# Kernel tuning notes

Hardware: AMD Instinct MI355X
Metric: run time of the kernel (lower is better)

The kernel has to match this reference:

```python
import jax, jax.numpy as jnp
import numpy as np
from jax import lax

EPS = 2e-5      # BatchNorm eps from source
TCLIP = 1.3     # FastSign STE clip


def fast_sign(x):
    # forward: sign(x); backward: grad of clamp(x, -1.3, 1.3) (straight-through)
    c = jnp.clip(x, -TCLIP, TCLIP)
    return lax.stop_gradient(jnp.sign(x) - c) + c


def conv2d(x, w, b, stride, pad):
    y = lax.conv_general_dilated(
        x, w, window_strides=stride,
        padding=[(pad[0], pad[0]), (pad[1], pad[1])],
        dimension_numbers=('NCHW', 'OIHW', 'NCHW'))
    return y + b[None, :, None, None]


def batchnorm(x, g, b):
    # training-mode BN: biased batch stats over (N, H, W)
    m = jnp.mean(x, axis=(0, 2, 3), keepdims=True)
    v = jnp.var(x, axis=(0, 2, 3), keepdims=True)
    return g[None, :, None, None] * (x - m) * lax.rsqrt(v + EPS) + b[None, :, None, None]


def maxpool3x3s2(x):
    return lax.reduce_window(x, -jnp.inf, lax.max, (1, 1, 3, 3), (1, 1, 2, 2), 'VALID')


def setup_inputs() -> dict:
    key = jax.random.key(0)
    ks = jax.random.split(key, 16)
    s = 0.05
    rn = lambda k, shape: jax.random.normal(k, shape, dtype=jnp.float32) * s
    NUM_CLASSES = 1000
    return {
        'x': jax.random.normal(ks[0], (8, 3, 211, 211), dtype=jnp.float32),
        'conv1_w': rn(ks[1], (96, 3, 11, 11)), 'conv1_b': rn(ks[2], (96,)),
        'bn1_g': jnp.ones((96,), jnp.float32), 'bn1_b': jnp.zeros((96,), jnp.float32),
        'conv2_w': rn(ks[3], (256, 96, 5, 5)), 'conv2_b': rn(ks[4], (256,)),
        'bn2_g': jnp.ones((256,), jnp.float32), 'bn2_b': jnp.zeros((256,), jnp.float32),
        'conv3_w': rn(ks[5], (384, 256, 3, 3)), 'conv3_b': rn(ks[6], (384,)),
        'bn3_g': jnp.ones((384,), jnp.float32), 'bn3_b': jnp.zeros((384,), jnp.float32),
        'conv4_w': rn(ks[7], (384, 384, 3, 3)), 'conv4_b': rn(ks[8], (384,)),
        'bn4_g': jnp.ones((384,), jnp.float32), 'bn4_b': jnp.zeros((384,), jnp.float32),
        'conv5_w': rn(ks[9], (256, 384, 3, 3)), 'conv5_b': rn(ks[10], (256,)),
        'bn5_g': jnp.ones((256,), jnp.float32), 'bn5_b': jnp.zeros((256,), jnp.float32),
        'fc1_w': rn(ks[11], (4096, 5)),
        'bn6_g': jnp.ones((256,), jnp.float32), 'bn6_b': jnp.zeros((256,), jnp.float32),
        'fc2_w': rn(ks[12], (4096, 4096)),
        'bn7_g': jnp.ones((256,), jnp.float32), 'bn7_b': jnp.zeros((256,), jnp.float32),
        'fc3_w': rn(ks[13], (NUM_CLASSES, 4096)), 'fc3_b': rn(ks[14], (NUM_CLASSES,)),
    }


def reference(x, conv1_w, conv1_b, bn1_g, bn1_b,
              conv2_w, conv2_b, bn2_g, bn2_b,
              conv3_w, conv3_b, bn3_g, bn3_b,
              conv4_w, conv4_b, bn4_g, bn4_b,
              conv5_w, conv5_b, bn5_g, bn5_b,
              fc1_w, bn6_g, bn6_b,
              fc2_w, bn7_g, bn7_b,
              fc3_w, fc3_b):
    # conv1 (full precision) + BN + relu + pool
    x = conv2d(x, conv1_w, conv1_b, (4, 4), (0, 0))           # [B,96,51,51]
    x = jax.nn.relu(batchnorm(x, bn1_g, bn1_b))
    x = maxpool3x3s2(x)                                        # [B,96,25,25]
    # binary conv blocks (act_q then BinaryConv2d binarizes input again, as in torch)
    x = fast_sign(x)
    x = conv2d(fast_sign(x), fast_sign(conv2_w), conv2_b, (1, 1), (2, 2))  # [B,256,25,25]
    x = batchnorm(x, bn2_g, bn2_b)
    x = maxpool3x3s2(x)                                        # [B,256,12,12]
    x = fast_sign(x)
    x = conv2d(fast_sign(x), fast_sign(conv3_w), conv3_b, (1, 1), (1, 1))  # [B,384,12,12]
    x = batchnorm(x, bn3_g, bn3_b)
    x = fast_sign(x)
    x = conv2d(fast_sign(x), fast_sign(conv4_w), conv4_b, (1, 1), (1, 1))
    x = batchnorm(x, bn4_g, bn4_b)
    x = fast_sign(x)
    x = conv2d(fast_sign(x), fast_sign(conv5_w), conv5_b, (1, 1), (1, 1))  # [B,256,12,12]
    x = batchnorm(x, bn5_g, bn5_b)
    x = maxpool3x3s2(x)                                        # [B,256,5,5]
    # fc layers applied on the LAST dim of the 4D tensor (faithful to torch F.linear)
    x = fast_sign(x)
    x = jnp.matmul(fast_sign(x), fast_sign(fc1_w).T)           # [B,256,5,4096]
    x = jax.nn.relu(batchnorm(x, bn6_g, bn6_b))
    x = fast_sign(x)
    x = jnp.matmul(fast_sign(x), fast_sign(fc2_w).T)           # [B,256,5,4096]
    x = jax.nn.relu(batchnorm(x, bn7_g, bn7_b))
    x = jnp.matmul(x, fc3_w.T) + fc3_b                         # [B,256,5,1000]
    return jax.nn.softmax(x, axis=1)                           # softmax over dim=1 (channels)
```

## Files before the change

kernel.cpp:

```cpp
#include <hip/hip_runtime.h>
#include <cstdint>
#include <cstddef>


typedef int      v4i  __attribute__((ext_vector_type(4)));
typedef float    v4f  __attribute__((ext_vector_type(4)));
typedef _Float16 v8h  __attribute__((ext_vector_type(8)));

#define EPS_BN 2e-5

__device__ __forceinline__ void g2l16(const void* g, void* l) {
  __builtin_amdgcn_global_load_lds((__attribute__((address_space(1))) void*)g,
                                   (__attribute__((address_space(3))) void*)l,
                                   16, 0, 0);
}

__global__ __launch_bounds__(256) void conv1_k(const float* __restrict__ x,
                                               const float* __restrict__ w,
                                               float* __restrict__ y) {
  const int bid = blockIdx.x;
  const int n = bid / 51, oh = bid % 51;
  const int tid = threadIdx.x, lane = tid & 63, wave = tid >> 6;
  __shared__ __align__(16) float xs[3 * 11 * 272];
  for (int i = tid; i < 3 * 11 * 272; i += 256) {
    int iw = i % 272;
    int t = i / 272;
    int kh = t % 11, ci = t / 11;
    float v = 0.f;
    if (iw < 211) v = x[((size_t)(n * 3 + ci) * 211 + (oh * 4 + kh)) * 211 + iw];
    xs[i] = v;
  }
  __syncthreads();
  const int ow = lane;
  const int g = blockIdx.y;
  {
    const int co0 = wave * 24 + g * 4;
    float a0 = 0.f, a1 = 0.f, a2 = 0.f, a3 = 0.f;
    for (int ci = 0; ci < 3; ++ci) {
#pragma unroll
      for (int kh = 0; kh < 11; ++kh) {
        const float* xr = xs + (ci * 11 + kh) * 272 + ow * 4;
        float4 q0 = *(const float4*)(xr);
        float4 q1 = *(const float4*)(xr + 4);
        float4 q2 = *(const float4*)(xr + 8);
        float xv[11] = {q0.x, q0.y, q0.z, q0.w, q1.x, q1.y,
                        q1.z, q1.w, q2.x, q2.y, q2.z};
        const float* wr = w + ((size_t)co0 * 3 + ci) * 121 + kh * 11;
#pragma unroll
        for (int kw = 0; kw < 11; ++kw) {
          float xvv = xv[kw];
          a0 = fmaf(xvv, wr[kw], a0);
          a1 = fmaf(xvv, wr[363 + kw], a1);
          a2 = fmaf(xvv, wr[726 + kw], a2);
          a3 = fmaf(xvv, wr[1089 + kw], a3);
        }
      }
    }
    if (ow < 51) {
      size_t ob = ((size_t)(n * 96 + co0) * 51 + oh) * 51 + ow;
      y[ob] = a0;
      y[ob + 2601] = a1;
      y[ob + 2 * 2601] = a2;
      y[ob + 3 * 2601] = a3;
    }
  }
}

template <typename T>
__global__ __launch_bounds__(256) void bnstat_nchw_k(const T* __restrict__ y,
                                                     const float* __restrict__ g,
                                                     const float* __restrict__ bb,
                                                     float* __restrict__ par,
                                                     int C, int HW, int Nn) {
  const int c = blockIdx.x;
  double s = 0.0, q = 0.0;
  for (int n = 0; n < Nn; ++n) {
    const T* p = y + ((size_t)n * C + c) * HW;
    for (int r = threadIdx.x; r < HW; r += 256) {
      double v = (double)p[r];
      s += v;
      q += v * v;
    }
  }
  __shared__ double ss[256], qq[256];
  ss[threadIdx.x] = s;
  qq[threadIdx.x] = q;
  __syncthreads();
  for (int st = 128; st > 0; st >>= 1) {
    if (threadIdx.x < st) {
      ss[threadIdx.x] += ss[threadIdx.x + st];
      qq[threadIdx.x] += qq[threadIdx.x + st];
    }
    __syncthreads();
  }
  if (threadIdx.x == 0) {
    double P = (double)Nn * HW;
    double m = ss[0] / P, var = qq[0] / P - m * m;
    float inv = (float)(1.0 / sqrt(var + EPS_BN));
    float sc = g[c] * inv;
    par[c] = sc;
    par[512 + c] = bb[c] - (float)m * sc;
  }
}

template <typename T>
__global__ __launch_bounds__(256) void bnstat_nhwc_k(const T* __restrict__ y,
                                                     const float* __restrict__ g,
                                                     const float* __restrict__ bb,
                                                     float* __restrict__ par,
                                                     int C, int P) {
  const int c = blockIdx.x;
  double s = 0.0, q = 0.0;
  for (int p = threadIdx.x; p < P; p += 256) {
    double v = (double)y[(size_t)p * C + c];
    s += v;
    q += v * v;
  }
  __shared__ double ss[256], qq[256];
  ss[threadIdx.x] = s;
  qq[threadIdx.x] = q;
  __syncthreads();
  for (int st = 128; st > 0; st >>= 1) {
    if (threadIdx.x < st) {
      ss[threadIdx.x] += ss[threadIdx.x + st];
      qq[threadIdx.x] += qq[threadIdx.x + st];
    }
    __syncthreads();
  }
  if (threadIdx.x == 0) {
    double Pd = (double)P;
    double m = ss[0] / Pd, var = qq[0] / Pd - m * m;
    float inv = (float)(1.0 / sqrt(var + EPS_BN));
    float sc = g[c] * inv;
    par[c] = sc;
    par[512 + c] = bb[c] - (float)m * sc;
  }
}

__global__ __launch_bounds__(256) void bnp16_k(const short* __restrict__ y,
                                               double* __restrict__ part) {
  const int c = blockIdx.x, n = blockIdx.y;
  const short* p = y + ((size_t)(n * 256 + c)) * 20480;
  long long s = 0, q = 0;
  for (int r = threadIdx.x; r < 20480; r += 256) {
    int v = p[r];
    s += v;
    q += (long long)v * v;
  }
  __shared__ long long ss[256], qq[256];
  ss[threadIdx.x] = s;
  qq[threadIdx.x] = q;
  __syncthreads();
  for (int st = 128; st > 0; st >>= 1) {
    if (threadIdx.x < st) {
      ss[threadIdx.x] += ss[threadIdx.x + st];
      qq[threadIdx.x] += qq[threadIdx.x + st];
    }
    __syncthreads();
  }
  if (threadIdx.x == 0) {
    part[(size_t)(n * 256 + c) * 2] = (double)ss[0];
    part[(size_t)(n * 256 + c) * 2 + 1] = (double)qq[0];
  }
}

__global__ __launch_bounds__(256) void bnf7_k(const double* __restrict__ part,
                                              const float* __restrict__ g,
                                              const float* __restrict__ bb,
                                              float* __restrict__ par) {
  int c = threadIdx.x;
  double s = 0.0, q = 0.0;
  for (int n = 0; n < 8; ++n) {
    s += part[(size_t)(n * 256 + c) * 2];
    q += part[(size_t)(n * 256 + c) * 2 + 1];
  }
  double P = 163840.0;
  double m = s / P, var = q / P - m * m;
  float inv = (float)(1.0 / sqrt(var + EPS_BN));
  float sc = g[c] * inv;
  par[c] = sc;
  par[512 + c] = bb[c] - (float)m * sc;
}

__global__ __launch_bounds__(256) void pool1sign_k(const float* __restrict__ y,
                                                   const float* __restrict__ par,
                                                   int8_t* __restrict__ o) {
  unsigned idx = blockIdx.x * 256 + threadIdx.x;
  if (idx >= 8u * 96 * 25 * 25) return;
  unsigned ow = idx % 25, t = idx / 25;
  unsigned oh = t % 25;
  t /= 25;
  unsigned c = t % 96, n = t / 96;
  float sc = par[c], sh = par[512 + c];
  const float* p = y + ((size_t)(n * 96 + c) * 51 + oh * 2) * 51 + ow * 2;
  float mx = -1e30f, mn = 1e30f;
#pragma unroll
  for (int kh = 0; kh < 3; ++kh)
#pragma unroll
    for (int kw = 0; kw < 3; ++kw) {
      float v = p[kh * 51 + kw];
      mx = fmaxf(mx, v);
      mn = fminf(mn, v);
    }
  float z = (sc >= 0.f ? sc * mx : sc * mn) + sh;
  o[((n * 25 + oh) * 25 + ow) * 96 + c] = (z > 0.f) ? 1 : 0;
}

__global__ __launch_bounds__(256) void poolsign_k(const short* __restrict__ y,
                                                  const float* __restrict__ par,
                                                  int8_t* __restrict__ o, int Nn,
                                                  int Hin, int C, int Hout) {
  unsigned idx = blockIdx.x * 256 + threadIdx.x;
  if (idx >= (unsigned)Nn * Hout * Hout * C) return;
  unsigned c = idx % C;
  unsigned t = idx / C;
  unsigned ow = t % Hout;
  t /= Hout;
  unsigned oh = t % Hout;
  unsigned n = t / Hout;
  const short* p = y + ((size_t)(n * Hin + oh * 2) * Hin + ow * 2) * C + c;
  int mx = -1000000, mn = 1000000;
#pragma unroll
  for (int kh = 0; kh < 3; ++kh)
#pragma unroll
    for (int kw = 0; kw < 3; ++kw) {
      int v = p[(kh * Hin + kw) * C];
      mx = max(mx, v);
      mn = min(mn, v);
    }
  float sc = par[c];
  float z = (sc >= 0.f ? sc * (float)mx : sc * (float)mn) + par[512 + c];
  o[idx] = (z > 0.f) ? 1 : ((z < 0.f) ? -1 : 0);
}

__global__ __launch_bounds__(256) void signk(const short* __restrict__ y,
                                             const float* __restrict__ par,
                                             int8_t* __restrict__ o, int total,
                                             int C) {
  unsigned idx = blockIdx.x * 256 + threadIdx.x;
  if (idx >= (unsigned)total) return;
  unsigned c = idx % C;
  float z = par[c] * (float)y[idx] + par[512 + c];
  o[idx] = (z > 0.f) ? 1 : ((z < 0.f) ? -1 : 0);
}

__global__ __launch_bounds__(256) void pool5sign_k(const short* __restrict__ y,
                                                   const float* __restrict__ par,
                                                   int8_t* __restrict__ o) {
  unsigned idx = blockIdx.x * 256 + threadIdx.x;
  if (idx >= 8u * 256 * 25) return;
  unsigned ow = idx % 5;
  unsigned t = idx / 5;
  unsigned oh = t % 5;
  t /= 5;
  unsigned c = t % 256, n = t / 256;
  const short* p = y + ((size_t)(n * 12 + oh * 2) * 12 + ow * 2) * 256 + c;
  int mx = -1000000, mn = 1000000;
#pragma unroll
  for (int kh = 0; kh < 3; ++kh)
#pragma unroll
    for (int kw = 0; kw < 3; ++kw) {
      int v = p[(kh * 12 + kw) * 256];
      mx = max(mx, v);
      mn = min(mn, v);
    }
  float sc = par[c];
  float z = (sc >= 0.f ? sc * (float)mx : sc * (float)mn) + par[512 + c];
  o[idx] = (z > 0.f) ? 1 : ((z < 0.f) ? -1 : 0);
}

__global__ __launch_bounds__(256) void quantw_k(const float* __restrict__ w,
                                                int8_t* __restrict__ o, int Co,
                                                int Ci, int KHW, int K, int Kp) {
  unsigned idx = blockIdx.x * 256 + threadIdx.x;
  if (idx >= (unsigned)Co * Kp) return;
  unsigned k = idx % Kp;
  unsigned co = idx / Kp;
  int8_t v = 0;
  if (k < (unsigned)K) {
    unsigned tap = k / Ci, ci = k - tap * Ci;
    float f = w[((size_t)co * Ci + ci) * KHW + tap];
    v = (f > 0.f) ? 1 : ((f < 0.f) ? -1 : 0);
  }
  o[idx] = v;
}

__global__ __launch_bounds__(256) void quantwv_k(const float* __restrict__ w,
                                                 int8_t* __restrict__ o,
                                                 unsigned total4) {
  unsigned idx = blockIdx.x * 256 + threadIdx.x;
  if (idx >= total4) return;
  float4 f = ((const float4*)w)[idx];
  union { int8_t b[4]; int i; } u;
  u.b[0] = (f.x > 0.f) ? 1 : ((f.x < 0.f) ? -1 : 0);
  u.b[1] = (f.y > 0.f) ? 1 : ((f.y < 0.f) ? -1 : 0);
  u.b[2] = (f.z > 0.f) ? 1 : ((f.z < 0.f) ? -1 : 0);
  u.b[3] = (f.w > 0.f) ? 1 : ((f.w < 0.f) ? -1 : 0);
  ((int*)o)[idx] = u.i;
}

__global__ __launch_bounds__(256) void im2colv_k(const int8_t* __restrict__ a,
                                                 int8_t* __restrict__ o, int Nn,
                                                 int H, int C, int KH, int pad,
                                                 int K, int Kp) {
  unsigned t = blockIdx.x * 256 + threadIdx.x;
  unsigned chunks = (unsigned)Kp >> 4;
  unsigned total = (unsigned)Nn * H * H * chunks;
  if (t >= total) return;
  unsigned kc = t % chunks;
  unsigned m = t / chunks;
  unsigned ow = m % H;
  unsigned tmp = m / H;
  unsigned oh = tmp % H;
  unsigned n = tmp / H;
  unsigned k0 = kc << 4;
  int4 v = {0, 0, 0, 0};
  if (k0 < (unsigned)K) {
    unsigned tap = k0 / C;
    unsigned ci = k0 - tap * C;
    unsigned kh = tap / KH, kw = tap - kh * KH;
    int ih = (int)oh - pad + (int)kh, iw = (int)ow - pad + (int)kw;
    if (ih >= 0 && ih < H && iw >= 0 && iw < H)
      v = *(const int4*)(a + (((n * H + ih) * H + iw) * C + ci));
  }
  *(int4*)(o + (size_t)m * Kp + k0) = v;
}

__global__ __launch_bounds__(256) void gemm_i8_k(const int8_t* __restrict__ A,
                                                 const int8_t* __restrict__ B,
                                                 short* __restrict__ Cm, int M,
                                                 int N, int Kp) {
  __shared__ __align__(16) int8_t As[128 * 64];
  __shared__ __align__(16) int8_t Bs[128 * 64];
  const int tid = threadIdx.x;
  const int lane = tid & 63, wave = tid >> 6;
  const int m0 = blockIdx.x * 128, n0 = blockIdx.y * 128;
  const int wm = (wave >> 1) * 64, wn = (wave & 1) * 64;
  v4i acc[4][4];
#pragma unroll
  for (int r = 0; r < 4; ++r)
#pragma unroll
    for (int u = 0; u < 4; ++u) acc[r][u] = (v4i){0, 0, 0, 0};

  int r_[2], g_[2];
#pragma unroll
  for (int q = 0; q < 2; ++q) {
    int idx = q * 256 + tid;
    r_[q] = idx >> 2;
    g_[q] = (((idx & 3) ^ ((r_[q] >> 1) & 3)) << 4);
  }
  int aoff[4], boff[4];
#pragma unroll
  for (int r = 0; r < 4; ++r) {
    int m = wm + r * 16 + (lane & 15);
    aoff[r] = m * 64 + (((lane >> 4) ^ ((m >> 1) & 3)) << 4);
    int n = wn + r * 16 + (lane & 15);
    boff[r] = n * 64 + (((lane >> 4) ^ ((n >> 1) & 3)) << 4);
  }

  for (int k0 = 0; k0 < Kp; k0 += 64) {
#pragma unroll
    for (int q = 0; q < 2; ++q) {
      int idx = q * 256 + tid;
      g2l16(A + (size_t)(m0 + r_[q]) * Kp + k0 + g_[q], As + idx * 16);
      g2l16(B + (size_t)(n0 + r_[q]) * Kp + k0 + g_[q], Bs + idx * 16);
    }
    __syncthreads();
    v4i af[4], bf[4];
#pragma unroll
    for (int r = 0; r < 4; ++r) {
      af[r] = *(const v4i*)(As + aoff[r]);
      bf[r] = *(const v4i*)(Bs + boff[r]);
    }
#pragma unroll
    for (int r = 0; r < 4; ++r)
#pragma unroll
      for (int u = 0; u < 4; ++u)
        acc[r][u] = __builtin_amdgcn_mfma_i32_16x16x64_i8(af[r], bf[u],
                                                          acc[r][u], 0, 0, 0);
    __syncthreads();
  }
  const int colD = lane & 15, rowD = (lane >> 4) * 4;
#pragma unroll
  for (int r = 0; r < 4; ++r)
#pragma unroll
    for (int u = 0; u < 4; ++u) {
      int n = n0 + wn + u * 16 + colD;
#pragma unroll
      for (int e = 0; e < 4; ++e) {
        int m = m0 + wm + r * 16 + rowD + e;
        if (m < M) Cm[(size_t)m * N + n] = (short)acc[r][u][e];
      }
    }
}

__global__ __launch_bounds__(256) void gemm_i8_64k(const int8_t* __restrict__ A,
                                                   const int8_t* __restrict__ B,
                                                   short* __restrict__ Cm, int M,
                                                   int N, int Kp) {
  __shared__ __align__(16) int8_t As[64 * 64];
  __shared__ __align__(16) int8_t Bs[64 * 64];
  const int tid = threadIdx.x;
  const int lane = tid & 63, wave = tid >> 6;
  const int m0 = blockIdx.x * 64, n0 = blockIdx.y * 64;
  const int wm = (wave >> 1) * 32, wn = (wave & 1) * 32;
  v4i acc[2][2];
#pragma unroll
  for (int r = 0; r < 2; ++r)
#pragma unroll
    for (int u = 0; u < 2; ++u) acc[r][u] = (v4i){0, 0, 0, 0};

  const int rs = tid >> 2;
  const int gsw = (((tid & 3) ^ ((rs >> 1) & 3)) << 4);
  int aoff[2], boff[2];
#pragma unroll
  for (int r = 0; r < 2; ++r) {
    int m = wm + r * 16 + (lane & 15);
    aoff[r] = m * 64 + (((lane >> 4) ^ ((m >> 1) & 3)) << 4);
    int n = wn + r * 16 + (lane & 15);
    boff[r] = n * 64 + (((lane >> 4) ^ ((n >> 1) & 3)) << 4);
  }

  for (int k0 = 0; k0 < Kp; k0 += 64) {
    g2l16(A + (size_t)(m0 + rs) * Kp + k0 + gsw, As + tid * 16);
    g2l16(B + (size_t)(n0 + rs) * Kp + k0 + gsw, Bs + tid * 16);
    __syncthreads();
    v4i af[2], bf[2];
#pragma unroll
    for (int r = 0; r < 2; ++r) {
      af[r] = *(const v4i*)(As + aoff[r]);
      bf[r] = *(const v4i*)(Bs + boff[r]);
    }
#pragma unroll
    for (int r = 0; r < 2; ++r)
#pragma unroll
      for (int u = 0; u < 2; ++u)
        acc[r][u] = __builtin_amdgcn_mfma_i32_16x16x64_i8(af[r], bf[u],
                                                          acc[r][u], 0, 0, 0);
    __syncthreads();
  }
  const int colD = lane & 15, rowD = (lane >> 4) * 4;
#pragma unroll
  for (int r = 0; r < 2; ++r)
#pragma unroll
    for (int u = 0; u < 2; ++u) {
      int n = n0 + wn + u * 16 + colD;
#pragma unroll
      for (int e = 0; e < 4; ++e) {
        int m = m0 + wm + r * 16 + rowD + e;
        if (m < M) Cm[(size_t)m * N + n] = (short)acc[r][u][e];
      }
    }
}

__global__ __launch_bounds__(256) void gemm_f16_k(const _Float16* __restrict__ A,
                                                  const _Float16* __restrict__ B,
                                                  float* __restrict__ out,
                                                  const float* __restrict__ bias,
                                                  int M, int Nout, int K) {
  __shared__ __align__(16) int8_t As[128 * 64];
  __shared__ __align__(16) int8_t Bs[128 * 64];
  const int tid = threadIdx.x;
  const int lane = tid & 63, wave = tid >> 6;
  const int m0 = blockIdx.x * 128, n0 = blockIdx.y * 128;
  const int wm = (wave >> 1) * 64, wn = (wave & 1) * 64;
  const int KpB = K * 2;
  v4f acc[4][4];
#pragma unroll
  for (int r = 0; r < 4; ++r)
#pragma unroll
    for (int u = 0; u < 4; ++u) acc[r][u] = (v4f){0.f, 0.f, 0.f, 0.f};

  int r_[2], g_[2];
#pragma unroll
  for (int q = 0; q < 2; ++q) {
    int idx = q * 256 + tid;
    r_[q] = idx >> 2;
    g_[q] = (((idx & 3) ^ ((r_[q] >> 1) & 3)) << 4);
  }
  int aoff[4], boff[4];
#pragma unroll
  for (int r = 0; r < 4; ++r) {
    int m = wm + r * 16 + (lane & 15);
    aoff[r] = m * 64 + (((lane >> 4) ^ ((m >> 1) & 3)) << 4);
    int n = wn + r * 16 + (lane & 15);
    boff[r] = n * 64 + (((lane >> 4) ^ ((n >> 1) & 3)) << 4);
  }

  const int8_t* Ab = (const int8_t*)A;
  const int8_t* Bb = (const int8_t*)B;
  for (int k0 = 0; k0 < KpB; k0 += 64) {
#pragma unroll
    for (int q = 0; q < 2; ++q) {
      int idx = q * 256 + tid;
      g2l16(Ab + (size_t)(m0 + r_[q]) * KpB + k0 + g_[q], As + idx * 16);
      g2l16(Bb + (size_t)(n0 + r_[q]) * KpB + k0 + g_[q], Bs + idx * 16);
    }
    __syncthreads();
    v8h af[4], bf[4];
#pragma unroll
    for (int r = 0; r < 4; ++r) {
      af[r] = *(const v8h*)(As + aoff[r]);
      bf[r] = *(const v8h*)(Bs + boff[r]);
    }
#pragma unroll
    for (int r = 0; r < 4; ++r)
#pragma unroll
      for (int u = 0; u < 4; ++u)
        acc[r][u] = __builtin_amdgcn_mfma_f32_16x16x32_f16(af[r], bf[u],
                                                           acc[r][u], 0, 0, 0);
    __syncthreads();
  }
  const int colD = lane & 15, rowD = (lane >> 4) * 4;
#pragma unroll
  for (int r = 0; r < 4; ++r)
#pragma unroll
    for (int u = 0; u < 4; ++u) {
      int n = n0 + wn + u * 16 + colD;
      if (n < Nout) {
        float bv = bias[n];
#pragma unroll
        for (int e = 0; e < 4; ++e) {
          int m = m0 + wm + r * 16 + rowD + e;
          if (m < M) out[(size_t)m * Nout + n] = acc[r][u][e] + bv;
        }
      }
    }
}

__global__ __launch_bounds__(256) void gram_k(const int8_t* __restrict__ wq1,
                                              int* __restrict__ gm) {
  __shared__ int sg[30];
  if (threadIdx.x < 30) sg[threadIdx.x] = 0;
  __syncthreads();
  int acc[30];
#pragma unroll
  for (int i = 0; i < 30; ++i) acc[i] = 0;
  for (int j = threadIdx.x; j < 4096; j += 256) {
    const int8_t* w = wq1 + j * 5;
    int v[5];
#pragma unroll
    for (int k = 0; k < 5; ++k) v[k] = w[k];
#pragma unroll
    for (int k = 0; k < 5; ++k) {
      acc[k] += v[k];
#pragma unroll
      for (int l = 0; l < 5; ++l) acc[5 + k * 5 + l] += v[k] * v[l];
    }
  }
#pragma unroll
  for (int i = 0; i < 30; ++i) atomicAdd(&sg[i], acc[i]);
  __syncthreads();
  if (threadIdx.x < 30) gm[threadIdx.x] = sg[threadIdx.x];
}

__global__ __launch_bounds__(256) void par6_k(const int8_t* __restrict__ s5,
                                              const int* __restrict__ gm,
                                              const float* __restrict__ g,
                                              const float* __restrict__ bb,
                                              float* __restrict__ par) {
  int c = threadIdx.x;
  long long s = 0, q = 0;
  for (int n = 0; n < 8; ++n)
    for (int i = 0; i < 5; ++i) {
      const int8_t* a = s5 + ((size_t)((n * 256 + c) * 5 + i)) * 5;
      int av[5];
#pragma unroll
      for (int k = 0; k < 5; ++k) av[k] = a[k];
      int ds = 0, dq = 0;
#pragma unroll
      for (int k = 0; k < 5; ++k) {
        ds += av[k] * gm[k];
#pragma unroll
        for (int l = 0; l < 5; ++l) dq += av[k] * av[l] * gm[5 + k * 5 + l];
      }
      s += ds;
      q += dq;
    }
  double P = 163840.0;
  double m = (double)s / P, var = (double)q / P - m * m;
  float inv = (float)(1.0 / sqrt(var + EPS_BN));
  float sc = g[c] * inv;
  par[c] = sc;
  par[512 + c] = bb[c] - (float)m * sc;
}

__global__ __launch_bounds__(256) void fc1f_k(const int8_t* __restrict__ s5,
                                              const int8_t* __restrict__ wq1,
                                              const float* __restrict__ par,
                                              int8_t* __restrict__ f1) {
  unsigned idx = blockIdx.x * 256 + threadIdx.x;
  if (idx >= 10240u * 256) return;
  unsigned m = idx >> 8, jg = idx & 255;
  unsigned c = (m / 5) & 255;
  float sc = par[c], sh = par[512 + c];
  const int8_t* ap = s5 + m * 5;
  int a0 = ap[0], a1 = ap[1], a2 = ap[2], a3 = ap[3], a4 = ap[4];
  int8_t wb[80];
  const int4* wp = (const int4*)(wq1 + jg * 80);
#pragma unroll
  for (int qq = 0; qq < 5; ++qq) *(int4*)(wb + qq * 16) = wp[qq];
  union { int8_t b[16]; int4 v; } ov;
#pragma unroll
  for (int t = 0; t < 16; ++t) {
    int d = a0 * wb[t * 5] + a1 * wb[t * 5 + 1] + a2 * wb[t * 5 + 2] +
            a3 * wb[t * 5 + 3] + a4 * wb[t * 5 + 4];
    float z = sc * (float)d + sh;
    ov.b[t] = (z > 0.f) ? 1 : 0;
  }
  *(int4*)(f1 + (size_t)m * 4096 + jg * 16) = ov.v;
}

__global__ __launch_bounds__(256) void x7v_k(short* __restrict__ f2,
                                             const float* __restrict__ par) {
  unsigned idx = blockIdx.x * 256 + threadIdx.x;
  if (idx >= 10240u * 4096 / 8) return;
  unsigned base8 = idx * 8;
  unsigned c = (base8 / 20480) & 255;
  float sc = par[c], sh = par[512 + c];
  union { int4 v; short s[8]; } in;
  in.v = *(int4*)(f2 + (size_t)base8);
  union { int4 v; _Float16 h[8]; } outv;
#pragma unroll
  for (int t = 0; t < 8; ++t) {
    float z = sc * (float)in.s[t] + sh;
    if (z < 0.f) z = 0.f;
    outv.h[t] = (_Float16)z;
  }
  *(int4*)((_Float16*)f2 + (size_t)base8) = outv.v;
}

__global__ __launch_bounds__(256) void w3h_k(const float* __restrict__ w,
                                             _Float16* __restrict__ o) {
  unsigned idx = blockIdx.x * 256 + threadIdx.x;
  if (idx >= 1024u * 4096) return;
  unsigned j = idx >> 12;
  o[idx] = (j < 1000) ? (_Float16)w[idx] : (_Float16)0.f;
}

__global__ __launch_bounds__(256) void softmax_k(float* __restrict__ o) {
  unsigned t = blockIdx.x * 256 + threadIdx.x;
  if (t >= 40000) return;
  unsigned j = t % 1000;
  unsigned i = (t / 1000) % 5;
  unsigned b = t / 5000;
  float* p = o + ((size_t)(b * 256) * 5 + i) * 1000 + j;
  float mx = -1e30f;
  for (int c = 0; c < 256; ++c) mx = fmaxf(mx, p[(size_t)c * 5000]);
  float s = 0.f;
  for (int c = 0; c < 256; ++c) s += expf(p[(size_t)c * 5000] - mx);
  float inv = 1.f / s;
  for (int c = 0; c < 256; ++c)
    p[(size_t)c * 5000] = expf(p[(size_t)c * 5000] - mx) * inv;
}

static inline unsigned gs(size_t n) { return (unsigned)((n + 255) / 256); }

extern "C" void kernel_launch(void* const* d_in, const int* in_sizes, int n_in,
                              void* d_out, int out_size, void* d_ws,
                              size_t ws_size, hipStream_t stream) {
  (void)in_sizes; (void)n_in; (void)out_size; (void)ws_size;
  const float* x    = (const float*)d_in[0];
  const float* w1   = (const float*)d_in[1];
  const float* bn1g = (const float*)d_in[3];
  const float* bn1b = (const float*)d_in[4];
  const float* w2   = (const float*)d_in[5];
  const float* bn2g = (const float*)d_in[7];
  const float* bn2b = (const float*)d_in[8];
  const float* w3   = (const float*)d_in[9];
  const float* bn3g = (const float*)d_in[11];
  const float* bn3b = (const float*)d_in[12];
  const float* w4   = (const float*)d_in[13];
  const float* bn4g = (const float*)d_in[15];
  const float* bn4b = (const float*)d_in[16];
  const float* w5   = (const float*)d_in[17];
  const float* bn5g = (const float*)d_in[19];
  const float* bn5b = (const float*)d_in[20];
  const float* fc1w = (const float*)d_in[21];
  const float* bn6g = (const float*)d_in[22];
  const float* bn6b = (const float*)d_in[23];
  const float* fc2w = (const float*)d_in[24];
  const float* bn7g = (const float*)d_in[25];
  const float* bn7b = (const float*)d_in[26];
  const float* fc3w = (const float*)d_in[27];
  const float* fc3b = (const float*)d_in[28];
  float* out = (float*)d_out;

  char* ws = (char*)d_ws;
  size_t off = 0;
  auto alloc = [&](size_t bytes) -> void* {
    off = (off + 255) & ~(size_t)255;
    void* p = ws + off;
    off += bytes;
    return p;
  };
  float*   Y1   = (float*)alloc((size_t)8 * 96 * 51 * 51 * 4);
  int8_t*  S1   = (int8_t*)alloc((size_t)8 * 25 * 25 * 96);
  int8_t*  IM   = (int8_t*)alloc((size_t)5120 * 2432);
  short*   Y2   = (short*)alloc((size_t)5056 * 256 * 2);
  int8_t*  S2   = (int8_t*)alloc((size_t)1152 * 256);
  short*   Y3   = (short*)alloc((size_t)1152 * 384 * 2);
  int8_t*  S3   = (int8_t*)alloc((size_t)1152 * 384);
  short*   Y4   = (short*)alloc((size_t)1152 * 384 * 2);
  int8_t*  S4   = (int8_t*)alloc((size_t)1152 * 384);
  short*   Y5   = (short*)alloc((size_t)1152 * 256 * 2);
  int8_t*  S5   = (int8_t*)alloc((size_t)8 * 256 * 25);
  int8_t*  WQ2  = (int8_t*)alloc((size_t)256 * 2432);
  int8_t*  WQ3  = (int8_t*)alloc((size_t)384 * 2304);
  int8_t*  WQ4  = (int8_t*)alloc((size_t)384 * 3456);
  int8_t*  WQ5  = (int8_t*)alloc((size_t)256 * 3456);
  int8_t*  WQ1  = (int8_t*)alloc((size_t)4096 * 5);
  int8_t*  WQF2 = (int8_t*)alloc((size_t)4096 * 4096);
  int8_t*  F1   = (int8_t*)alloc((size_t)10240 * 4096);
  short*   F2   = (short*)alloc((size_t)10240 * 4096 * 2);
  _Float16* W3H = (_Float16*)alloc((size_t)1024 * 4096 * 2);
  float*   PAR  = (float*)alloc((size_t)7 * 1024 * 4);
  int*     GM   = (int*)alloc(32 * 4);
  double*  PART = (double*)alloc((size_t)2048 * 2 * 8);
  float* par1 = PAR;
  float* par2 = PAR + 1024;
  float* par3 = PAR + 2048;
  float* par4 = PAR + 3072;
  float* par5 = PAR + 4096;
  float* par6 = PAR + 5120;
  float* par7 = PAR + 6144;

  quantw_k<<<gs((size_t)256 * 2432), 256, 0, stream>>>(w2, WQ2, 256, 96, 25, 2400, 2432);
  quantw_k<<<gs((size_t)384 * 2304), 256, 0, stream>>>(w3, WQ3, 384, 256, 9, 2304, 2304);
  quantw_k<<<gs((size_t)384 * 3456), 256, 0, stream>>>(w4, WQ4, 384, 384, 9, 3456, 3456);
  quantw_k<<<gs((size_t)256 * 3456), 256, 0, stream>>>(w5, WQ5, 256, 384, 9, 3456, 3456);
  quantw_k<<<gs((size_t)4096 * 5), 256, 0, stream>>>(fc1w, WQ1, 4096, 5, 1, 5, 5);
  quantwv_k<<<gs((size_t)4096 * 1024), 256, 0, stream>>>(fc2w, WQF2, 4096u * 1024);
  w3h_k<<<gs((size_t)1024 * 4096), 256, 0, stream>>>(fc3w, W3H);

  conv1_k<<<dim3(8 * 51, 6), 256, 0, stream>>>(x, w1, Y1);
  bnstat_nchw_k<float><<<dim3(96), 256, 0, stream>>>(Y1, bn1g, bn1b, par1, 96, 2601, 8);
  pool1sign_k<<<gs((size_t)8 * 96 * 625), 256, 0, stream>>>(Y1, par1, S1);

  im2colv_k<<<gs((size_t)5000 * 152), 256, 0, stream>>>(S1, IM, 8, 25, 96, 5, 2, 2400, 2432);
  gemm_i8_64k<<<dim3(79, 4), 256, 0, stream>>>(IM, WQ2, Y2, 5000, 256, 2432);
  bnstat_nhwc_k<short><<<dim3(256), 256, 0, stream>>>(Y2, bn2g, bn2b, par2, 256, 5000);
  poolsign_k<<<gs((size_t)8 * 144 * 256), 256, 0, stream>>>(Y2, par2, S2, 8, 25, 256, 12);

  im2colv_k<<<gs((size_t)1152 * 144), 256, 0, stream>>>(S2, IM, 8, 12, 256, 3, 1, 2304, 2304);
  gemm_i8_64k<<<dim3(18, 6), 256, 0, stream>>>(IM, WQ3, Y3, 1152, 384, 2304);
  bnstat_nhwc_k<short><<<dim3(384), 256, 0, stream>>>(Y3, bn3g, bn3b, par3, 384, 1152);
  signk<<<gs((size_t)1152 * 384), 256, 0, stream>>>(Y3, par3, S3, 1152 * 384, 384);

  im2colv_k<<<gs((size_t)1152 * 216), 256, 0, stream>>>(S3, IM, 8, 12, 384, 3, 1, 3456, 3456);
  gemm_i8_64k<<<dim3(18, 6), 256, 0, stream>>>(IM, WQ4, Y4, 1152, 384, 3456);
  bnstat_nhwc_k<short><<<dim3(384), 256, 0, stream>>>(Y4, bn4g, bn4b, par4, 384, 1152);
  signk<<<gs((size_t)1152 * 384), 256, 0, stream>>>(Y4, par4, S4, 1152 * 384, 384);

  im2colv_k<<<gs((size_t)1152 * 216), 256, 0, stream>>>(S4, IM, 8, 12, 384, 3, 1, 3456, 3456);
  gemm_i8_64k<<<dim3(18, 4), 256, 0, stream>>>(IM, WQ5, Y5, 1152, 256, 3456);
  bnstat_nhwc_k<short><<<dim3(256), 256, 0, stream>>>(Y5, bn5g, bn5b, par5, 256, 1152);
  pool5sign_k<<<gs((size_t)8 * 256 * 25), 256, 0, stream>>>(Y5, par5, S5);

  gram_k<<<dim3(1), 256, 0, stream>>>(WQ1, GM);
  par6_k<<<dim3(1), 256, 0, stream>>>(S5, GM, bn6g, bn6b, par6);
  fc1f_k<<<gs((size_t)10240 * 256), 256, 0, stream>>>(S5, WQ1, par6, F1);

  gemm_i8_k<<<dim3(80, 32), 256, 0, stream>>>(F1, WQF2, F2, 10240, 4096, 4096);
  bnp16_k<<<dim3(256, 8), 256, 0, stream>>>(F2, PART);
  bnf7_k<<<dim3(1), 256, 0, stream>>>(PART, bn7g, bn7b, par7);
  x7v_k<<<gs((size_t)10240 * 512), 256, 0, stream>>>(F2, par7);

  gemm_f16_k<<<dim3(80, 8), 256, 0, stream>>>((const _Float16*)F2, W3H, out, fc3b,
                                              10240, 1000, 4096);
  softmax_k<<<gs(40000), 256, 0, stream>>>(out);
}
```

Measured before the change: 1.099 ms.

## Widen GEMM N tiles to 256 and restructure softmax via shared-memory tiles

Both the int8 fc2 GEMM and the f16 fc3 GEMM now use 128x256 block tiles, each wave owning 64x128, which doubles accumulator registers and B-tile LDS. The aim is more MFMA work per A-tile load and half as many blocks. Separately, softmax is rewritten so each block stages a 256x32 channel tile in LDS and does block-cooperative max and sum reductions, instead of each thread making three strided global passes over 256 channels. The larger accumulator footprint may cut occupancy or cause register spills, and with 1000 outputs the fc3 GEMM wastes more padded columns in its last tile.

```diff
diff --git a/kernel.cpp b/kernel.cpp
--- a/kernel.cpp
+++ b/kernel.cpp
@@ -331,31 +331,35 @@
                                                  short* __restrict__ Cm, int M,
                                                  int N, int Kp) {
   __shared__ __align__(16) int8_t As[128 * 64];
-  __shared__ __align__(16) int8_t Bs[128 * 64];
+  __shared__ __align__(16) int8_t Bs[256 * 64];
   const int tid = threadIdx.x;
   const int lane = tid & 63, wave = tid >> 6;
-  const int m0 = blockIdx.x * 128, n0 = blockIdx.y * 128;
-  const int wm = (wave >> 1) * 64, wn = (wave & 1) * 64;
-  v4i acc[4][4];
+  const int m0 = blockIdx.x * 128, n0 = blockIdx.y * 256;
+  const int wm = (wave >> 1) * 64, wn = (wave & 1) * 128;
+  v4i acc[4][8];
 #pragma unroll
   for (int r = 0; r < 4; ++r)
 #pragma unroll
-    for (int u = 0; u < 4; ++u) acc[r][u] = (v4i){0, 0, 0, 0};
-
-  int r_[2], g_[2];
-#pragma unroll
-  for (int q = 0; q < 2; ++q) {
+    for (int u = 0; u < 8; ++u) acc[r][u] = (v4i){0, 0, 0, 0};
+
+  int r_[6], g_[6];
+#pragma unroll
+  for (int q = 0; q < 6; ++q) {
     int idx = q * 256 + tid;
-    r_[q] = idx >> 2;
-    g_[q] = (((idx & 3) ^ ((r_[q] >> 1) & 3)) << 4);
-  }
-  int aoff[4], boff[4];
+    int row = idx >> 2;
+    r_[q] = (q < 2) ? row : (row - 128);
+    g_[q] = (((idx & 3) ^ ((row >> 1) & 3)) << 4);
+  }
+  int aoff[4], boff[8];
 #pragma unroll
   for (int r = 0; r < 4; ++r) {
     int m = wm + r * 16 + (lane & 15);
     aoff[r] = m * 64 + (((lane >> 4) ^ ((m >> 1) & 3)) << 4);
-    int n = wn + r * 16 + (lane & 15);
-    boff[r] = n * 64 + (((lane >> 4) ^ ((n >> 1) & 3)) << 4);
+  }
+#pragma unroll
+  for (int u = 0; u < 8; ++u) {
+    int n = wn + u * 16 + (lane & 15);
+    boff[u] = n * 64 + (((lane >> 4) ^ ((n >> 1) & 3)) << 4);
   }
 
   for (int k0 = 0; k0 < Kp; k0 += 64) {
@@ -363,19 +367,22 @@
     for (int q = 0; q < 2; ++q) {
       int idx = q * 256 + tid;
       g2l16(A + (size_t)(m0 + r_[q]) * Kp + k0 + g_[q], As + idx * 16);
-      g2l16(B + (size_t)(n0 + r_[q]) * Kp + k0 + g_[q], Bs + idx * 16);
+    }
+#pragma unroll
+    for (int q = 2; q < 6; ++q) {
+      int idx = q * 256 + tid;
+      g2l16(B + (size_t)(n0 + r_[q]) * Kp + k0 + g_[q], Bs + (idx - 512) * 16);
     }
     __syncthreads();
-    v4i af[4], bf[4];
-#pragma unroll
-    for (int r = 0; r < 4; ++r) {
-      af[r] = *(const v4i*)(As + aoff[r]);
-      bf[r] = *(const v4i*)(Bs + boff[r]);
-    }
+    v4i af[4], bf[8];
+#pragma unroll
+    for (int r = 0; r < 4; ++r) af[r] = *(const v4i*)(As + aoff[r]);
+#pragma unroll
+    for (int u = 0; u < 8; ++u) bf[u] = *(const v4i*)(Bs + boff[u]);
 #pragma unroll
     for (int r = 0; r < 4; ++r)
 #pragma unroll
-      for (int u = 0; u < 4; ++u)
+      for (int u = 0; u < 8; ++u)
         acc[r][u] = __builtin_amdgcn_mfma_i32_16x16x64_i8(af[r], bf[u],
                                                           acc[r][u], 0, 0, 0);
     __syncthreads();
@@ -384,7 +391,7 @@
 #pragma unroll
   for (int r = 0; r < 4; ++r)
 #pragma unroll
-    for (int u = 0; u < 4; ++u) {
+    for (int u = 0; u < 8; ++u) {
       int n = n0 + wn + u * 16 + colD;
 #pragma unroll
       for (int e = 0; e < 4; ++e) {
@@ -459,32 +466,36 @@
                                                   const float* __restrict__ bias,
                                                   int M, int Nout, int K) {
   __shared__ __align__(16) int8_t As[128 * 64];
-  __shared__ __align__(16) int8_t Bs[128 * 64];
+  __shared__ __align__(16) int8_t Bs[256 * 64];
   const int tid = threadIdx.x;
   const int lane = tid & 63, wave = tid >> 6;
-  const int m0 = blockIdx.x * 128, n0 = blockIdx.y * 128;
-  const int wm = (wave >> 1) * 64, wn = (wave & 1) * 64;
+  const int m0 = blockIdx.x * 128, n0 = blockIdx.y * 256;
+  const int wm = (wave >> 1) * 64, wn = (wave & 1) * 128;
   const int KpB = K * 2;
-  v4f acc[4][4];
+  v4f acc[4][8];
 #pragma unroll
   for (int r = 0; r < 4; ++r)
 #pragma unroll
-    for (int u = 0; u < 4; ++u) acc[r][u] = (v4f){0.f, 0.f, 0.f, 0.f};
-
-  int r_[2], g_[2];
-#pragma unroll
-  for (int q = 0; q < 2; ++q) {
+    for (int u = 0; u < 8; ++u) acc[r][u] = (v4f){0.f, 0.f, 0.f, 0.f};
+
+  int r_[6], g_[6];
+#pragma unroll
+  for (int q = 0; q < 6; ++q) {
     int idx = q * 256 + tid;
-    r_[q] = idx >> 2;
-    g_[q] = (((idx & 3) ^ ((r_[q] >> 1) & 3)) << 4);
-  }
-  int aoff[4], boff[4];
+    int row = idx >> 2;
+    r_[q] = (q < 2) ? row : (row - 128);
+    g_[q] = (((idx & 3) ^ ((row >> 1) & 3)) << 4);
+  }
+  int aoff[4], boff[8];
 #pragma unroll
   for (int r = 0; r < 4; ++r) {
     int m = wm + r * 16 + (lane & 15);
     aoff[r] = m * 64 + (((lane >> 4) ^ ((m >> 1) & 3)) << 4);
-    int n = wn + r * 16 + (lane & 15);
-    boff[r] = n * 64 + (((lane >> 4) ^ ((n >> 1) & 3)) << 4);
+  }
+#pragma unroll
+  for (int u = 0; u < 8; ++u) {
+    int n = wn + u * 16 + (lane & 15);
+    boff[u] = n * 64 + (((lane >> 4) ^ ((n >> 1) & 3)) << 4);
   }
 
   const int8_t* Ab = (const int8_t*)A;
@@ -494,19 +505,22 @@
     for (int q = 0; q < 2; ++q) {
       int idx = q * 256 + tid;
       g2l16(Ab + (size_t)(m0 + r_[q]) * KpB + k0 + g_[q], As + idx * 16);
-      g2l16(Bb + (size_t)(n0 + r_[q]) * KpB + k0 + g_[q], Bs + idx * 16);
+    }
+#pragma unroll
+    for (int q = 2; q < 6; ++q) {
+      int idx = q * 256 + tid;
+      g2l16(Bb + (size_t)(n0 + r_[q]) * KpB + k0 + g_[q], Bs + (idx - 512) * 16);
     }
     __syncthreads();
-    v8h af[4], bf[4];
-#pragma unroll
-    for (int r = 0; r < 4; ++r) {
-      af[r] = *(const v8h*)(As + aoff[r]);
-      bf[r] = *(const v8h*)(Bs + boff[r]);
-    }
+    v8h af[4], bf[8];
+#pragma unroll
+    for (int r = 0; r < 4; ++r) af[r] = *(const v8h*)(As + aoff[r]);
+#pragma unroll
+    for (int u = 0; u < 8; ++u) bf[u] = *(const v8h*)(Bs + boff[u]);
 #pragma unroll
     for (int r = 0; r < 4; ++r)
 #pragma unroll
-      for (int u = 0; u < 4; ++u)
+      for (int u = 0; u < 8; ++u)
         acc[r][u] = __builtin_amdgcn_mfma_f32_16x16x32_f16(af[r], bf[u],
                                                            acc[r][u], 0, 0, 0);
     __syncthreads();
@@ -515,7 +529,7 @@
 #pragma unroll
   for (int r = 0; r < 4; ++r)
 #pragma unroll
-    for (int u = 0; u < 4; ++u) {
+    for (int u = 0; u < 8; ++u) {
       int n = n0 + wn + u * 16 + colD;
       if (n < Nout) {
         float bv = bias[n];
@@ -639,19 +653,52 @@
 }
 
 __global__ __launch_bounds__(256) void softmax_k(float* __restrict__ o) {
-  unsigned t = blockIdx.x * 256 + threadIdx.x;
-  if (t >= 40000) return;
-  unsigned j = t % 1000;
-  unsigned i = (t / 1000) % 5;
-  unsigned b = t / 5000;
-  float* p = o + ((size_t)(b * 256) * 5 + i) * 1000 + j;
-  float mx = -1e30f;
-  for (int c = 0; c < 256; ++c) mx = fmaxf(mx, p[(size_t)c * 5000]);
-  float s = 0.f;
-  for (int c = 0; c < 256; ++c) s += expf(p[(size_t)c * 5000] - mx);
-  float inv = 1.f / s;
-  for (int c = 0; c < 256; ++c)
-    p[(size_t)c * 5000] = expf(p[(size_t)c * 5000] - mx) * inv;
+  __shared__ float tile[256][33];
+  __shared__ float red[8][32];
+  __shared__ float mxs[32], invs[32];
+  const int bi = blockIdx.x;
+  const int jt = blockIdx.y;
+  const int b = bi / 5, i = bi % 5;
+  float* base = o + ((size_t)(b * 256) * 5 + i) * 1000;
+  const int t = threadIdx.x;
+  const int jl = t & 31, part = t >> 5;
+  const int j = jt * 32 + jl;
+  const bool ok = (j < 1000);
+  for (int cg = 0; cg < 32; ++cg) {
+    int c = cg * 8 + part;
+    tile[c][jl] = ok ? base[(size_t)c * 5000 + j] : 0.f;
+  }
+  __syncthreads();
+  float pm = -1e30f;
+#pragma unroll 4
+  for (int cc = 0; cc < 32; ++cc) pm = fmaxf(pm, tile[part * 32 + cc][jl]);
+  red[part][jl] = pm;
+  __syncthreads();
+  if (part == 0) {
+    float m = red[0][jl];
+#pragma unroll
+    for (int p = 1; p < 8; ++p) m = fmaxf(m, red[p][jl]);
+    mxs[jl] = m;
+  }
+  __syncthreads();
+  float mx = mxs[jl];
+  float ps = 0.f;
+#pragma unroll 4
+  for (int cc = 0; cc < 32; ++cc) ps += expf(tile[part * 32 + cc][jl] - mx);
+  red[part][jl] = ps;
+  __syncthreads();
+  if (part == 0) {
+    float s = red[0][jl];
+#pragma unroll
+    for (int p = 1; p < 8; ++p) s += red[p][jl];
+    invs[jl] = 1.f / s;
+  }
+  __syncthreads();
+  float inv = invs[jl];
+  for (int cg = 0; cg < 32; ++cg) {
+    int c = cg * 8 + part;
+    if (ok) base[(size_t)c * 5000 + j] = expf(tile[c][jl] - mx) * inv;
+  }
 }
 
 static inline unsigned gs(size_t n) { return (unsigned)((n + 255) / 256); }
@@ -761,12 +808,12 @@
   par6_k<<<dim3(1), 256, 0, stream>>>(S5, GM, bn6g, bn6b, par6);
   fc1f_k<<<gs((size_t)10240 * 256), 256, 0, stream>>>(S5, WQ1, par6, F1);
 
-  gemm_i8_k<<<dim3(80, 32), 256, 0, stream>>>(F1, WQF2, F2, 10240, 4096, 4096);
+  gemm_i8_k<<<dim3(80, 16), 256, 0, stream>>>(F1, WQF2, F2, 10240, 4096, 4096);
   bnp16_k<<<dim3(256, 8), 256, 0, stream>>>(F2, PART);
   bnf7_k<<<dim3(1), 256, 0, stream>>>(PART, bn7g, bn7b, par7);
   x7v_k<<<gs((size_t)10240 * 512), 256, 0, stream>>>(F2, par7);
 
-  gemm_f16_k<<<dim3(80, 8), 256, 0, stream>>>((const _Float16*)F2, W3H, out, fc3b,
+  gemm_f16_k<<<dim3(80, 4), 256, 0, stream>>>((const _Float16*)F2, W3H, out, fc3b,
                                               10240, 1000, 4096);
-  softmax_k<<<gs(40000), 256, 0, stream>>>(out);
-}
+  softmax_k<<<dim3(40, 32), 256, 0, stream>>>(out);
+}
```

After: 1.213 ms. +10.3%, slower.
